# Kernel optimization log

Measured on AMD Instinct MI355X. Metric: run time of the kernel, lower is better.

## Reference

```python
import jax, jax.numpy as jnp
import numpy as np

DM, H, DK = 768, 12, 64

def setup_inputs() -> dict:
    key = jax.random.key(0)
    ks = jax.random.split(key, 12)
    B, S = 6, 1024
    sc = 1.0 / np.sqrt(DM)
    return {
        "Q": jax.random.normal(ks[0], (B, S, DM), jnp.float32),
        "K": jax.random.normal(ks[1], (B, S, DM), jnp.float32),
        "V": jax.random.normal(ks[2], (B, S, DM), jnp.float32),
        "attn_mask": jax.random.randint(ks[3], (B, S, S), 0, 2) > 0,
        "W_q": jax.random.uniform(ks[4], (DM, H * DK), jnp.float32, -sc, sc),
        "b_q": jax.random.uniform(ks[5], (H * DK,), jnp.float32, -sc, sc),
        "W_k": jax.random.uniform(ks[6], (DM, H * DK), jnp.float32, -sc, sc),
        "b_k": jax.random.uniform(ks[7], (H * DK,), jnp.float32, -sc, sc),
        "W_v": jax.random.uniform(ks[8], (DM, H * DK), jnp.float32, -sc, sc),
        "b_v": jax.random.uniform(ks[9], (H * DK,), jnp.float32, -sc, sc),
        "W_o": jax.random.uniform(ks[10], (H * DK, DM), jnp.float32, -1/np.sqrt(H*DK), 1/np.sqrt(H*DK)),
        "b_o": jax.random.uniform(ks[11], (DM,), jnp.float32, -1/np.sqrt(H*DK), 1/np.sqrt(H*DK)),
        "gamma": jnp.ones((DM,), jnp.float32),
        "beta": jnp.zeros((DM,), jnp.float32),
    }

def reference(Q, K, V, attn_mask, W_q, b_q, W_k, b_k, W_v, b_v, W_o, b_o, gamma, beta):
    B, S, _ = Q.shape
    residual = Q
    # projections -> [B, H, S, DK]
    q = (Q @ W_q + b_q).reshape(B, S, H, DK).transpose(0, 2, 1, 3)
    k = (K @ W_k + b_k).reshape(B, S, H, DK).transpose(0, 2, 1, 3)
    v = (V @ W_v + b_v).reshape(B, S, H, DK).transpose(0, 2, 1, 3)
    scores = jnp.einsum('bhqd,bhkd->bhqk', q, k) / np.sqrt(DK)
    scores = jnp.where(attn_mask[:, None, :, :], -1e9, scores)
    attn = jax.nn.softmax(scores, axis=-1)
    context = jnp.einsum('bhqk,bhkd->bhqd', attn, v)
    context = context.transpose(0, 2, 1, 3).reshape(B, S, H * DK)
    output = context @ W_o + b_o
    x = output + residual
    mu = jnp.mean(x, axis=-1, keepdims=True)
    var = jnp.var(x, axis=-1, keepdims=True)
    out = (x - mu) / jnp.sqrt(var + 1e-5) * gamma + beta
    return out, attn
```

## Files before the change

### kernel.cpp

```cpp
#include <hip/hip_runtime.h>
#include <hip/hip_bf16.h>

#define B 6
#define S 1024
#define H 12
#define DK 64
#define DM 768
#define M (B*S)
#define BH (B*H)

typedef __bf16 bf16;
typedef __attribute__((ext_vector_type(8))) __bf16 bf16x8;
typedef __attribute__((ext_vector_type(4))) float f32x4;

#define MFMA __builtin_amdgcn_mfma_f32_16x16x32_bf16
#define SFENCE() __builtin_amdgcn_sched_barrier(0)
#define WAITV(N) asm volatile("s_waitcnt vmcnt(" #N ")" ::: "memory")
#define BARRIER() __builtin_amdgcn_s_barrier()

__device__ __forceinline__ void gl16(const void* g, void* l) {
  __builtin_amdgcn_global_load_lds(
      (const __attribute__((address_space(1))) unsigned int*)g,
      (__attribute__((address_space(3))) unsigned int*)l, 16, 0, 0);
}

__global__ void k_prep(const float* __restrict__ Q, const float* __restrict__ K,
                       const float* __restrict__ V,
                       const float* __restrict__ Wq, const float* __restrict__ Wk,
                       const float* __restrict__ Wv, const float* __restrict__ Wo,
                       bf16* __restrict__ xb, bf16* __restrict__ wt) {
  int z = blockIdx.y;
  if (z < 3) {
    const float* X = z==0?Q : z==1?K : V;
    size_t i = ((size_t)blockIdx.x*256 + threadIdx.x)*8;
    float4 a = *(const float4*)(X + i);
    float4 b = *(const float4*)(X + i + 4);
    bf16x8 r;
    r[0]=(bf16)a.x; r[1]=(bf16)a.y; r[2]=(bf16)a.z; r[3]=(bf16)a.w;
    r[4]=(bf16)b.x; r[5]=(bf16)b.y; r[6]=(bf16)b.z; r[7]=(bf16)b.w;
    *(bf16x8*)(xb + (size_t)z*M*DM + i) = r;
  } else {
    int zz = z - 3;
    const float* W = zz==0?Wq : zz==1?Wk : zz==2?Wv : Wo;
    int idx = blockIdx.x*256 + threadIdx.x;
    int k = idx / DM, n = idx % DM;
    wt[(size_t)zz*DM*DM + (size_t)n*DM + k] = (bf16)W[idx];
  }
}


__global__ __launch_bounds__(256, 3) void k_proj(
    const bf16* __restrict__ xb, const bf16* __restrict__ wt,
    const float* __restrict__ bq, const float* __restrict__ bk,
    const float* __restrict__ bv,
    bf16* __restrict__ qb, bf16* __restrict__ kb, bf16* __restrict__ vt) {
  int z = blockIdx.z;
  const bf16* X    = xb + (size_t)z*M*DM;
  const float* bias = z==0?bq : z==1?bk : bv;
  const bf16* Wt = wt + (size_t)z*DM*DM;
  int tid = threadIdx.x, lane = tid & 63, w = tid >> 6;
  int wr = w >> 1, wc = w & 1;
  int lr = lane & 15, lg = lane >> 4;
  int m0 = blockIdx.x*128;
  int n0 = blockIdx.y*128;

  __shared__ bf16 As[3][4096];
  __shared__ bf16 Bs[3][4096];
  char* AsL = (char*)&As[0][0];
  char* BsL = (char*)&Bs[0][0];

  const int r1 = tid >> 2, p1 = tid & 3;
  const int s1 = p1 ^ ((r1 >> 1) & 3);
  const bf16* a1 = X  + (size_t)(m0 + r1)*DM      + s1*8;
  const bf16* a2 = X  + (size_t)(m0 + r1 + 64)*DM + s1*8;
  const bf16* b1 = Wt + (size_t)(n0 + r1)*DM      + s1*8;
  const bf16* b2 = Wt + (size_t)(n0 + r1 + 64)*DM + s1*8;
  const int ldsOff = w*1024;

  const int fs = (lr >> 1) & 3;
  const int fchunk = (lg ^ fs) * 8;

  f32x4 acc[4][4];
  #pragma unroll
  for (int i=0;i<4;++i)
    #pragma unroll
    for (int j=0;j<4;++j) acc[i][j] = (f32x4){0.f,0.f,0.f,0.f};

  #pragma unroll
  for (int tt = 0; tt < 2; ++tt) {
    gl16(a1 + tt*32, AsL + tt*8192 + ldsOff);
    gl16(a2 + tt*32, AsL + tt*8192 + 4096 + ldsOff);
    gl16(b1 + tt*32, BsL + tt*8192 + ldsOff);
    gl16(b2 + tt*32, BsL + tt*8192 + 4096 + ldsOff);
  }
  SFENCE();
  WAITV(4);
  BARRIER();
  SFENCE();

  int cur = 0, nb = 2;
  for (int t = 0; t < 24; ++t) {
    const bf16* Ac = (const bf16*)(AsL + cur*8192);
    const bf16* Bc = (const bf16*)(BsL + cur*8192);
    if (t < 22) {
      int k0 = (t+2)*32;
      gl16(a1 + k0, AsL + nb*8192 + ldsOff);
      gl16(a2 + k0, AsL + nb*8192 + 4096 + ldsOff);
      gl16(b1 + k0, BsL + nb*8192 + ldsOff);
      gl16(b2 + k0, BsL + nb*8192 + 4096 + ldsOff);
    }
    SFENCE();
    bf16x8 af[4], bfr[4];
    __builtin_amdgcn_s_setprio(1);
    #pragma unroll
    for (int mi=0;mi<4;++mi) af[mi]  = *(const bf16x8*)&Ac[(wr*64 + mi*16 + lr)*32 + fchunk];
    #pragma unroll
    for (int ni=0;ni<4;++ni) bfr[ni] = *(const bf16x8*)&Bc[(wc*64 + ni*16 + lr)*32 + fchunk];
    #pragma unroll
    for (int mi=0;mi<4;++mi)
      #pragma unroll
      for (int ni=0;ni<4;++ni)
        acc[mi][ni] = MFMA(af[mi], bfr[ni], acc[mi][ni], 0,0,0);
    __builtin_amdgcn_s_setprio(0);
    SFENCE();
    if (t < 23) {
      if (t < 22) { WAITV(4); } else { WAITV(0); }
      BARRIER();
      SFENCE();
    }
    cur = (cur==2)?0:cur+1;
    nb  = (nb==2)?0:nb+1;
  }

  int mw = m0 + wr*64, nw = n0 + wc*64;
  #pragma unroll
  for (int ni=0;ni<4;++ni) {
    int n = nw + ni*16 + lr;
    float bs = bias[n];
    int h = n >> 6, d = n & 63;
    #pragma unroll
    for (int mi=0;mi<4;++mi)
      #pragma unroll
      for (int r=0;r<4;++r) {
        int m = mw + mi*16 + lg*4 + r;
        int bb = m >> 10, s = m & 1023;
        float val = acc[mi][ni][r] + bs;
        if (z == 0) {
          qb[((size_t)(bb*H + h)*S + s)*DK + d] = (bf16)val;
        } else if (z == 1) {
          int dsw = ((((d>>3) ^ (s&7))) << 3) | (d&7);
          kb[((size_t)(bb*H + h)*S + s)*DK + dsw] = (bf16)val;
        } else {
          int ssw = (s & ~63) | ((((s&63)>>3) ^ (d&7)) << 3) | (s&7);
          vt[((size_t)(bb*H + h)*DK + d)*S + ssw] = (bf16)val;
        }
      }
  }
}

__global__ __launch_bounds__(256, 3) void k_oproj(
    const bf16* __restrict__ ctx, const bf16* __restrict__ wto,
    const float* __restrict__ bo, const float* __restrict__ res,
    float* __restrict__ x) {
  int tid = threadIdx.x, lane = tid & 63, w = tid >> 6;
  int wr = w >> 1, wc = w & 1;
  int lr = lane & 15, lg = lane >> 4;
  int m0 = blockIdx.x*128;
  int n0 = blockIdx.y*128;

  __shared__ bf16 As[3][4096];
  __shared__ bf16 Bs[3][4096];
  char* AsL = (char*)&As[0][0];
  char* BsL = (char*)&Bs[0][0];

  const int r1 = tid >> 2, p1 = tid & 3;
  const int s1 = p1 ^ ((r1 >> 1) & 3);
  const bf16* a1 = ctx + (size_t)(m0 + r1)*DM      + s1*8;
  const bf16* a2 = ctx + (size_t)(m0 + r1 + 64)*DM + s1*8;
  const bf16* b1 = wto + (size_t)(n0 + r1)*DM      + s1*8;
  const bf16* b2 = wto + (size_t)(n0 + r1 + 64)*DM + s1*8;
  const int ldsOff = w*1024;

  const int fs = (lr >> 1) & 3;
  const int fchunk = (lg ^ fs) * 8;

  f32x4 acc[4][4];
  #pragma unroll
  for (int i=0;i<4;++i)
    #pragma unroll
    for (int j=0;j<4;++j) acc[i][j] = (f32x4){0.f,0.f,0.f,0.f};

  #pragma unroll
  for (int tt = 0; tt < 2; ++tt) {
    gl16(a1 + tt*32, AsL + tt*8192 + ldsOff);
    gl16(a2 + tt*32, AsL + tt*8192 + 4096 + ldsOff);
    gl16(b1 + tt*32, BsL + tt*8192 + ldsOff);
    gl16(b2 + tt*32, BsL + tt*8192 + 4096 + ldsOff);
  }
  SFENCE();
  WAITV(4);
  BARRIER();
  SFENCE();

  int cur = 0, nb = 2;
  for (int t = 0; t < 24; ++t) {
    const bf16* Ac = (const bf16*)(AsL + cur*8192);
    const bf16* Bc = (const bf16*)(BsL + cur*8192);
    if (t < 22) {
      int k0 = (t+2)*32;
      gl16(a1 + k0, AsL + nb*8192 + ldsOff);
      gl16(a2 + k0, AsL + nb*8192 + 4096 + ldsOff);
      gl16(b1 + k0, BsL + nb*8192 + ldsOff);
      gl16(b2 + k0, BsL + nb*8192 + 4096 + ldsOff);
    }
    SFENCE();
    bf16x8 af[4], bfr[4];
    __builtin_amdgcn_s_setprio(1);
    #pragma unroll
    for (int mi=0;mi<4;++mi) af[mi]  = *(const bf16x8*)&Ac[(wr*64 + mi*16 + lr)*32 + fchunk];
    #pragma unroll
    for (int ni=0;ni<4;++ni) bfr[ni] = *(const bf16x8*)&Bc[(wc*64 + ni*16 + lr)*32 + fchunk];
    #pragma unroll
    for (int mi=0;mi<4;++mi)
      #pragma unroll
      for (int ni=0;ni<4;++ni)
        acc[mi][ni] = MFMA(af[mi], bfr[ni], acc[mi][ni], 0,0,0);
    __builtin_amdgcn_s_setprio(0);
    SFENCE();
    if (t < 23) {
      if (t < 22) { WAITV(4); } else { WAITV(0); }
      BARRIER();
      SFENCE();
    }
    cur = (cur==2)?0:cur+1;
    nb  = (nb==2)?0:nb+1;
  }

  int mw = m0 + wr*64, nw = n0 + wc*64;
  #pragma unroll
  for (int ni=0;ni<4;++ni) {
    int n = nw + ni*16 + lr;
    float bb = bo[n];
    #pragma unroll
    for (int mi=0;mi<4;++mi)
      #pragma unroll
      for (int r=0;r<4;++r) {
        int m = mw + mi*16 + lg*4 + r;
        x[(size_t)m*DM + n] = acc[mi][ni][r] + bb + res[(size_t)m*DM + n];
      }
  }
}

__device__ __forceinline__ unsigned pk2(float a, float b) {
  union { bf16 h[2]; unsigned u; } x;
  x.h[0] = (bf16)a; x.h[1] = (bf16)b;
  return x.u;
}

__global__ __launch_bounds__(256, 4) void k_fattn(
    const bf16* __restrict__ qb, const bf16* __restrict__ kb,
    const bf16* __restrict__ vt, const unsigned char* __restrict__ mask,
    float* __restrict__ attn, bf16* __restrict__ ctx) {
  int lin = blockIdx.x + 16*blockIdx.y;
  int xcd  = lin & 7;
  int slot = lin >> 3;
  int qt   = slot & 15;
  int bh   = xcd*9 + (slot >> 4);
  int b = bh / H, h = bh - b*H;
  int tid = threadIdx.x, lane = tid & 63, w = tid >> 6;
  int lr = lane & 15, lg = lane >> 4;
  int q0 = qt*64 + w*16;

  __shared__ bf16 Kb[2][4096];
  __shared__ bf16 Vb[2][4096];
  __shared__ bf16 pt[4][512];
  char* KbL = (char*)&Kb[0][0];
  char* VbL = (char*)&Vb[0][0];

  const bf16* qbase = qb + ((size_t)bh*S + q0 + lr)*DK + lg*8;
  bf16x8 qa0 = *(const bf16x8*)(qbase);
  bf16x8 qa1 = *(const bf16x8*)(qbase + 32);
  SFENCE();

  const char* kg = (const char*)(kb + (size_t)bh*S*DK);
  const char* vg = (const char*)(vt + (size_t)bh*DK*S);
  const unsigned char* mrow = mask + ((size_t)b*S + q0 + lr)*S;
  float* abase = attn + ((size_t)bh*S + q0 + lr)*S;

  const char* ksrc  = kg + w*2048 + lane*16;
  const char* vsrcA = vg + (size_t)(w*16 + (lane>>3))*2048 + (lane&7)*16;
  const char* vsrcB = vsrcA + 8*2048;
  const int ldsK = w*2048;

  const int krow = lr*64;
  const int kf0o = krow + ((lg ^ (lr&7))<<3);
  const int kf1o = krow + (((4+lg) ^ (lr&7))<<3);
  const int swzP = (lr & 3) << 4;

  uchar4 mkc[4], mkn[4];

  gl16(ksrc,        KbL + ldsK);
  gl16(ksrc + 1024, KbL + ldsK + 1024);
  SFENCE();
  #pragma unroll
  for (int i=0;i<4;++i) mkn[i] = *(const uchar4*)(mrow + i*16 + lg*4);
  SFENCE();
  WAITV(4);
  BARRIER();
  SFENCE();

  float sum = 0.f;
  for (int t = 0; t < 16; ++t) {
    const bf16* Kc = (const bf16*)(KbL + (t&1)*8192);
    if (t < 15) {
      gl16(ksrc + (t+1)*8192,        KbL + ((t+1)&1)*8192 + ldsK);
      gl16(ksrc + (t+1)*8192 + 1024, KbL + ((t+1)&1)*8192 + ldsK + 1024);
    }
    SFENCE();
    #pragma unroll
    for (int i=0;i<4;++i) mkc[i] = mkn[i];
    if (t < 15) {
      #pragma unroll
      for (int i=0;i<4;++i) mkn[i] = *(const uchar4*)(mrow + (t+1)*64 + i*16 + lg*4);
    }
    __builtin_amdgcn_s_setprio(1);
    #pragma unroll
    for (int i=0;i<4;++i) {
      bf16x8 kf0 = *(const bf16x8*)&Kc[i*1024 + kf0o];
      bf16x8 kf1 = *(const bf16x8*)&Kc[i*1024 + kf1o];
      f32x4 sc = {0.f,0.f,0.f,0.f};
      sc = MFMA(kf0, qa0, sc, 0,0,0);
      sc = MFMA(kf1, qa1, sc, 0,0,0);
      sum += mkc[i].x ? 0.f : __expf(sc[0]*0.125f);
      sum += mkc[i].y ? 0.f : __expf(sc[1]*0.125f);
      sum += mkc[i].z ? 0.f : __expf(sc[2]*0.125f);
      sum += mkc[i].w ? 0.f : __expf(sc[3]*0.125f);
    }
    __builtin_amdgcn_s_setprio(0);
    SFENCE();
    if (t < 15) {
      WAITV(4);
      BARRIER();
      SFENCE();
    }
  }
  sum += __shfl_xor(sum, 16);
  sum += __shfl_xor(sum, 32);
  float inv = 1.f / sum;

  f32x4 cacc[4];
  #pragma unroll
  for (int d=0;d<4;++d) cacc[d] = (f32x4){0.f,0.f,0.f,0.f};

  gl16(ksrc,        KbL + ldsK);
  gl16(ksrc + 1024, KbL + ldsK + 1024);
  gl16(vsrcA,       VbL + ldsK);
  gl16(vsrcB,       VbL + ldsK + 1024);
  SFENCE();
  #pragma unroll
  for (int i=0;i<4;++i) mkn[i] = *(const uchar4*)(mrow + i*16 + lg*4);
  SFENCE();
  WAITV(4);
  BARRIER();
  SFENCE();

  for (int t = 0; t < 16; ++t) {
    const bf16* Kc = (const bf16*)(KbL + (t&1)*8192);
    const bf16* Vc = (const bf16*)(VbL + (t&1)*8192);
    if (t < 15) {
      gl16(ksrc + (t+1)*8192,        KbL + ((t+1)&1)*8192 + ldsK);
      gl16(ksrc + (t+1)*8192 + 1024, KbL + ((t+1)&1)*8192 + ldsK + 1024);
      gl16(vsrcA + (t+1)*128,        VbL + ((t+1)&1)*8192 + ldsK);
      gl16(vsrcB + (t+1)*128,        VbL + ((t+1)&1)*8192 + ldsK + 1024);
    }
    SFENCE();
    #pragma unroll
    for (int i=0;i<4;++i) mkc[i] = mkn[i];
    if (t < 15) {
      #pragma unroll
      for (int i=0;i<4;++i) mkn[i] = *(const uchar4*)(mrow + (t+1)*64 + i*16 + lg*4);
    }
    char* buf = (char*)&pt[w][0];
    __builtin_amdgcn_s_setprio(1);
    #pragma unroll
    for (int u = 0; u < 2; ++u) {
      #pragma unroll
      for (int half = 0; half < 2; ++half) {
        int i = u*2 + half;
        bf16x8 kf0 = *(const bf16x8*)&Kc[i*1024 + kf0o];
        bf16x8 kf1 = *(const bf16x8*)&Kc[i*1024 + kf1o];
        f32x4 sc = {0.f,0.f,0.f,0.f};
        sc = MFMA(kf0, qa0, sc, 0,0,0);
        sc = MFMA(kf1, qa1, sc, 0,0,0);
        float p0 = mkc[i].x ? 0.f : __expf(sc[0]*0.125f)*inv;
        float p1 = mkc[i].y ? 0.f : __expf(sc[1]*0.125f)*inv;
        float p2 = mkc[i].z ? 0.f : __expf(sc[2]*0.125f)*inv;
        float p3 = mkc[i].w ? 0.f : __expf(sc[3]*0.125f)*inv;
        *(float4*)(abase + t*64 + i*16 + lg*4) = (float4){p0,p1,p2,p3};
        uint2 pw2; pw2.x = pk2(p0,p1); pw2.y = pk2(p2,p3);
        *(uint2*)(buf + lr*64 + ((half*32 + lg*8) ^ swzP)) = pw2;
      }
      bf16x8 pa = *(const bf16x8*)(buf + lr*64 + ((lg*16) ^ swzP));
      #pragma unroll
      for (int dd=0; dd<4; ++dd) {
        bf16x8 vf = *(const bf16x8*)&Vc[dd*1024 + lr*64 + ((((u*4+lg) ^ (lr&7)))<<3)];
        cacc[dd] = MFMA(pa, vf, cacc[dd], 0,0,0);
      }
    }
    __builtin_amdgcn_s_setprio(0);
    SFENCE();
    if (t < 15) {
      WAITV(8);
      BARRIER();
      SFENCE();
    }
  }

  #pragma unroll
  for (int d=0;d<4;++d)
    #pragma unroll
    for (int r=0;r<4;++r)
      ctx[((size_t)b*S + q0 + lg*4 + r)*DM + h*DK + d*16 + lr] = (bf16)cacc[d][r];
}

__global__ void k_ln(const float* __restrict__ x, const float* __restrict__ gamma,
                     const float* __restrict__ beta, float* __restrict__ out) {
  int row = blockIdx.x; int tid = threadIdx.x;
  const float* xr = x + (size_t)row*DM;
  float v0 = xr[tid], v1 = xr[tid+256], v2 = xr[tid+512];
  float s = v0+v1+v2, ss = v0*v0+v1*v1+v2*v2;
  #pragma unroll
  for (int off=32; off; off>>=1){ s += __shfl_xor(s,off); ss += __shfl_xor(ss,off); }
  __shared__ float sm[8];
  int w = tid>>6;
  if ((tid&63)==0){ sm[w]=s; sm[4+w]=ss; }
  __syncthreads();
  s = sm[0]+sm[1]+sm[2]+sm[3]; ss = sm[4]+sm[5]+sm[6]+sm[7];
  float mean = s * (1.f/DM);
  float var = ss * (1.f/DM) - mean*mean;
  float rstd = rsqrtf(var + 1e-5f);
  out[(size_t)row*DM + tid]     = (v0-mean)*rstd*gamma[tid]     + beta[tid];
  out[(size_t)row*DM + tid+256] = (v1-mean)*rstd*gamma[tid+256] + beta[tid+256];
  out[(size_t)row*DM + tid+512] = (v2-mean)*rstd*gamma[tid+512] + beta[tid+512];
}

extern "C" void kernel_launch(void* const* d_in, const int* in_sizes, int n_in,
                              void* d_out, int out_size, void* d_ws, size_t ws_size,
                              hipStream_t stream) {
  const float* Q  = (const float*)d_in[0];
  const float* K  = (const float*)d_in[1];
  const float* V  = (const float*)d_in[2];
  const unsigned char* mask = (const unsigned char*)d_in[3];
  const float* Wq = (const float*)d_in[4];
  const float* bq = (const float*)d_in[5];
  const float* Wk = (const float*)d_in[6];
  const float* bk = (const float*)d_in[7];
  const float* Wv = (const float*)d_in[8];
  const float* bv = (const float*)d_in[9];
  const float* Wo = (const float*)d_in[10];
  const float* bo = (const float*)d_in[11];
  const float* gamma = (const float*)d_in[12];
  const float* beta  = (const float*)d_in[13];

  char* ws = (char*)d_ws;
  bf16* wt  = (bf16*)(ws + 0);
  bf16* xb  = (bf16*)(ws + 4718592);
  bf16* qb  = (bf16*)(ws + 33030144);
  bf16* kb  = (bf16*)(ws + 42467328);
  bf16* vt  = (bf16*)(ws + 51904512);
  bf16* ctx = (bf16*)(ws + 61341696);
  float* x  = (float*)(ws + 4718592);

  float* out  = (float*)d_out;
  float* attn = out + (size_t)B*S*DM;

  k_prep  <<<dim3(2304,7),  256, 0, stream>>>(Q,K,V,Wq,Wk,Wv,Wo,xb,wt);
  k_proj  <<<dim3(48,6,3),  256, 0, stream>>>(xb,wt,bq,bk,bv,qb,kb,vt);
  k_fattn <<<dim3(16,BH),   256, 0, stream>>>(qb,kb,vt,mask,attn,ctx);
  k_oproj <<<dim3(48,6),    256, 0, stream>>>(ctx, wt + (size_t)3*DM*DM, bo, Q, x);
  k_ln    <<<dim3(M),       256, 0, stream>>>(x,gamma,beta,out);
}
```

Before: 260.5 us.

## Fuse two-pass softmax attention into a single pass with deferred normalization

Replaces the two-pass attention (a sum pass, then a recompute-and-write pass) with one pass. Unnormalized exp probabilities are written to the attn output and accumulated into the context, and both are scaled by 1/sum afterwards. V fragments are now loaded straight from global memory into registers and double-buffered there instead of being staged in LDS. This removes the second QK^T and exp recompute and the second K stream, but adds a read-modify-write over the whole fp32 attn matrix and extra register pressure. It also drops max subtraction in exp, the same as the original code.

```diff
diff --git a/kernel.cpp b/kernel.cpp
--- a/kernel.cpp
+++ b/kernel.cpp
@@ -257,6 +257,53 @@
   return x.u;
 }
 
+#define FITER(T, P, VC, VN, MC, MN)                                           \
+  {                                                                           \
+    const bf16* Kc = (const bf16*)(KbL + (P)*8192);                           \
+    if ((T) < 15) {                                                           \
+      gl16(ksrc + ((T)+1)*8192,        KbL + ((P)^1)*8192 + ldsK);            \
+      gl16(ksrc + ((T)+1)*8192 + 1024, KbL + ((P)^1)*8192 + ldsK + 1024);     \
+    }                                                                         \
+    SFENCE();                                                                 \
+    if ((T) < 15) {                                                           \
+      _Pragma("unroll")                                                       \
+      for (int j=0;j<8;++j)                                                   \
+        VN[j] = *(const bf16x8*)(vg + voff[j] + ((T)+1)*128);                 \
+      _Pragma("unroll")                                                       \
+      for (int i=0;i<4;++i)                                                   \
+        MN[i] = *(const uchar4*)(mrow + ((T)+1)*64 + i*16 + lg*4);            \
+    }                                                                         \
+    SFENCE();                                                                 \
+    __builtin_amdgcn_s_setprio(1);                                            \
+    _Pragma("unroll")                                                         \
+    for (int u = 0; u < 2; ++u) {                                             \
+      _Pragma("unroll")                                                       \
+      for (int half = 0; half < 2; ++half) {                                  \
+        int i = u*2 + half;                                                   \
+        bf16x8 kf0 = *(const bf16x8*)&Kc[i*1024 + kf0o];                      \
+        bf16x8 kf1 = *(const bf16x8*)&Kc[i*1024 + kf1o];                      \
+        f32x4 sc = {0.f,0.f,0.f,0.f};                                         \
+        sc = MFMA(kf0, qa0, sc, 0,0,0);                                       \
+        sc = MFMA(kf1, qa1, sc, 0,0,0);                                       \
+        float p0 = MC[i].x ? 0.f : __expf(sc[0]*0.125f);                      \
+        float p1 = MC[i].y ? 0.f : __expf(sc[1]*0.125f);                      \
+        float p2 = MC[i].z ? 0.f : __expf(sc[2]*0.125f);                      \
+        float p3 = MC[i].w ? 0.f : __expf(sc[3]*0.125f);                      \
+        sum += p0 + p1 + p2 + p3;                                             \
+        *(float4*)(abase + (T)*64 + i*16 + lg*4) = (float4){p0,p1,p2,p3};     \
+        uint2 pw2; pw2.x = pk2(p0,p1); pw2.y = pk2(p2,p3);                    \
+        *(uint2*)(buf + lr*64 + ((half*32 + lg*8) ^ swzP)) = pw2;             \
+      }                                                                       \
+      bf16x8 pa = *(const bf16x8*)(buf + lr*64 + ((lg*16) ^ swzP));           \
+      _Pragma("unroll")                                                       \
+      for (int dd=0; dd<4; ++dd)                                              \
+        cacc[dd] = MFMA(pa, VC[u*4+dd], cacc[dd], 0,0,0);                     \
+    }                                                                         \
+    __builtin_amdgcn_s_setprio(0);                                            \
+    SFENCE();                                                                 \
+    if ((T) < 15) { WAITV(16); BARRIER(); SFENCE(); }                         \
+  }
+
 __global__ __launch_bounds__(256, 4) void k_fattn(
     const bf16* __restrict__ qb, const bf16* __restrict__ kb,
     const bf16* __restrict__ vt, const unsigned char* __restrict__ mask,
@@ -272,10 +319,8 @@
   int q0 = qt*64 + w*16;
 
   __shared__ bf16 Kb[2][4096];
-  __shared__ bf16 Vb[2][4096];
   __shared__ bf16 pt[4][512];
   char* KbL = (char*)&Kb[0][0];
-  char* VbL = (char*)&Vb[0][0];
 
   const bf16* qbase = qb + ((size_t)bh*S + q0 + lr)*DK + lg*8;
   bf16x8 qa0 = *(const bf16x8*)(qbase);
@@ -287,140 +332,71 @@
   const unsigned char* mrow = mask + ((size_t)b*S + q0 + lr)*S;
   float* abase = attn + ((size_t)bh*S + q0 + lr)*S;
 
-  const char* ksrc  = kg + w*2048 + lane*16;
-  const char* vsrcA = vg + (size_t)(w*16 + (lane>>3))*2048 + (lane&7)*16;
-  const char* vsrcB = vsrcA + 8*2048;
+  const char* ksrc = kg + w*2048 + lane*16;
   const int ldsK = w*2048;
+
+  int voff[8];
+  #pragma unroll
+  for (int u=0;u<2;++u)
+    #pragma unroll
+    for (int dd=0;dd<4;++dd)
+      voff[u*4+dd] = (dd*16+lr)*2048 + ((((u*4+lg) ^ (lr&7))) << 4);
 
   const int krow = lr*64;
   const int kf0o = krow + ((lg ^ (lr&7))<<3);
   const int kf1o = krow + (((4+lg) ^ (lr&7))<<3);
   const int swzP = (lr & 3) << 4;
 
-  uchar4 mkc[4], mkn[4];
-
   gl16(ksrc,        KbL + ldsK);
   gl16(ksrc + 1024, KbL + ldsK + 1024);
   SFENCE();
-  #pragma unroll
-  for (int i=0;i<4;++i) mkn[i] = *(const uchar4*)(mrow + i*16 + lg*4);
-  SFENCE();
-  WAITV(4);
+  bf16x8 vnA[8], vnB[8];
+  uchar4 mkA[4], mkB[4];
+  #pragma unroll
+  for (int j=0;j<8;++j) vnA[j] = *(const bf16x8*)(vg + voff[j]);
+  #pragma unroll
+  for (int i=0;i<4;++i) mkA[i] = *(const uchar4*)(mrow + i*16 + lg*4);
+  SFENCE();
+  WAITV(12);
   BARRIER();
   SFENCE();
 
+  f32x4 cacc[4];
+  #pragma unroll
+  for (int d=0;d<4;++d) cacc[d] = (f32x4){0.f,0.f,0.f,0.f};
   float sum = 0.f;
-  for (int t = 0; t < 16; ++t) {
-    const bf16* Kc = (const bf16*)(KbL + (t&1)*8192);
-    if (t < 15) {
-      gl16(ksrc + (t+1)*8192,        KbL + ((t+1)&1)*8192 + ldsK);
-      gl16(ksrc + (t+1)*8192 + 1024, KbL + ((t+1)&1)*8192 + ldsK + 1024);
-    }
-    SFENCE();
-    #pragma unroll
-    for (int i=0;i<4;++i) mkc[i] = mkn[i];
-    if (t < 15) {
-      #pragma unroll
-      for (int i=0;i<4;++i) mkn[i] = *(const uchar4*)(mrow + (t+1)*64 + i*16 + lg*4);
-    }
-    __builtin_amdgcn_s_setprio(1);
-    #pragma unroll
-    for (int i=0;i<4;++i) {
-      bf16x8 kf0 = *(const bf16x8*)&Kc[i*1024 + kf0o];
-      bf16x8 kf1 = *(const bf16x8*)&Kc[i*1024 + kf1o];
-      f32x4 sc = {0.f,0.f,0.f,0.f};
-      sc = MFMA(kf0, qa0, sc, 0,0,0);
-      sc = MFMA(kf1, qa1, sc, 0,0,0);
-      sum += mkc[i].x ? 0.f : __expf(sc[0]*0.125f);
-      sum += mkc[i].y ? 0.f : __expf(sc[1]*0.125f);
-      sum += mkc[i].z ? 0.f : __expf(sc[2]*0.125f);
-      sum += mkc[i].w ? 0.f : __expf(sc[3]*0.125f);
-    }
-    __builtin_amdgcn_s_setprio(0);
-    SFENCE();
-    if (t < 15) {
-      WAITV(4);
-      BARRIER();
-      SFENCE();
-    }
-  }
+  char* buf = (char*)&pt[w][0];
+
+  for (int tp = 0; tp < 8; ++tp) {
+    int t0 = tp*2;
+    FITER(t0,   0, vnA, vnB, mkA, mkB);
+    FITER(t0+1, 1, vnB, vnA, mkB, mkA);
+  }
+
   sum += __shfl_xor(sum, 16);
   sum += __shfl_xor(sum, 32);
   float inv = 1.f / sum;
-
-  f32x4 cacc[4];
-  #pragma unroll
-  for (int d=0;d<4;++d) cacc[d] = (f32x4){0.f,0.f,0.f,0.f};
-
-  gl16(ksrc,        KbL + ldsK);
-  gl16(ksrc + 1024, KbL + ldsK + 1024);
-  gl16(vsrcA,       VbL + ldsK);
-  gl16(vsrcB,       VbL + ldsK + 1024);
-  SFENCE();
-  #pragma unroll
-  for (int i=0;i<4;++i) mkn[i] = *(const uchar4*)(mrow + i*16 + lg*4);
-  SFENCE();
-  WAITV(4);
-  BARRIER();
-  SFENCE();
-
-  for (int t = 0; t < 16; ++t) {
-    const bf16* Kc = (const bf16*)(KbL + (t&1)*8192);
-    const bf16* Vc = (const bf16*)(VbL + (t&1)*8192);
-    if (t < 15) {
-      gl16(ksrc + (t+1)*8192,        KbL + ((t+1)&1)*8192 + ldsK);
-      gl16(ksrc + (t+1)*8192 + 1024, KbL + ((t+1)&1)*8192 + ldsK + 1024);
-      gl16(vsrcA + (t+1)*128,        VbL + ((t+1)&1)*8192 + ldsK);
-      gl16(vsrcB + (t+1)*128,        VbL + ((t+1)&1)*8192 + ldsK + 1024);
+  float invq[4];
+  #pragma unroll
+  for (int r=0;r<4;++r) invq[r] = __shfl(inv, lg*4 + r);
+  #pragma unroll
+  for (int d=0;d<4;++d)
+    #pragma unroll
+    for (int r=0;r<4;++r)
+      ctx[((size_t)b*S + q0 + lg*4 + r)*DM + h*DK + d*16 + lr] =
+          (bf16)(cacc[d][r] * invq[r]);
+
+  asm volatile("s_waitcnt vmcnt(0)" ::: "memory");
+  #pragma unroll 2
+  for (int t2 = 0; t2 < 16; ++t2) {
+    #pragma unroll
+    for (int i=0;i<4;++i) {
+      float4* p = (float4*)(abase + t2*64 + i*16 + lg*4);
+      float4 v = *p;
+      v.x*=inv; v.y*=inv; v.z*=inv; v.w*=inv;
+      *p = v;
     }
-    SFENCE();
-    #pragma unroll
-    for (int i=0;i<4;++i) mkc[i] = mkn[i];
-    if (t < 15) {
-      #pragma unroll
-      for (int i=0;i<4;++i) mkn[i] = *(const uchar4*)(mrow + (t+1)*64 + i*16 + lg*4);
-    }
-    char* buf = (char*)&pt[w][0];
-    __builtin_amdgcn_s_setprio(1);
-    #pragma unroll
-    for (int u = 0; u < 2; ++u) {
-      #pragma unroll
-      for (int half = 0; half < 2; ++half) {
-        int i = u*2 + half;
-        bf16x8 kf0 = *(const bf16x8*)&Kc[i*1024 + kf0o];
-        bf16x8 kf1 = *(const bf16x8*)&Kc[i*1024 + kf1o];
-        f32x4 sc = {0.f,0.f,0.f,0.f};
-        sc = MFMA(kf0, qa0, sc, 0,0,0);
-        sc = MFMA(kf1, qa1, sc, 0,0,0);
-        float p0 = mkc[i].x ? 0.f : __expf(sc[0]*0.125f)*inv;
-        float p1 = mkc[i].y ? 0.f : __expf(sc[1]*0.125f)*inv;
-        float p2 = mkc[i].z ? 0.f : __expf(sc[2]*0.125f)*inv;
-        float p3 = mkc[i].w ? 0.f : __expf(sc[3]*0.125f)*inv;
-        *(float4*)(abase + t*64 + i*16 + lg*4) = (float4){p0,p1,p2,p3};
-        uint2 pw2; pw2.x = pk2(p0,p1); pw2.y = pk2(p2,p3);
-        *(uint2*)(buf + lr*64 + ((half*32 + lg*8) ^ swzP)) = pw2;
-      }
-      bf16x8 pa = *(const bf16x8*)(buf + lr*64 + ((lg*16) ^ swzP));
-      #pragma unroll
-      for (int dd=0; dd<4; ++dd) {
-        bf16x8 vf = *(const bf16x8*)&Vc[dd*1024 + lr*64 + ((((u*4+lg) ^ (lr&7)))<<3)];
-        cacc[dd] = MFMA(pa, vf, cacc[dd], 0,0,0);
-      }
-    }
-    __builtin_amdgcn_s_setprio(0);
-    SFENCE();
-    if (t < 15) {
-      WAITV(8);
-      BARRIER();
-      SFENCE();
-    }
-  }
-
-  #pragma unroll
-  for (int d=0;d<4;++d)
-    #pragma unroll
-    for (int r=0;r<4;++r)
-      ctx[((size_t)b*S + q0 + lg*4 + r)*DM + h*DK + d*16 + lr] = (bf16)cacc[d][r];
+  }
 }
 
 __global__ void k_ln(const float* __restrict__ x, const float* __restrict__ gamma,
```

New measurement: 624.0 us. 140% more time.
